# Kernel tuning notes

Measured on AMD Instinct MI355X. Metric: run time of the kernel, lower is better.

Reference implementation:

```python
import jax, jax.numpy as jnp
import numpy as np

NUM_CODES = 8192
DIM = 256
TAU = 1.0
KL_WEIGHT = 0.01
COMMIT_WEIGHT = 0.25
B, C, P = 8, 64, 32


def setup_inputs() -> dict:
    key = jax.random.key(0)
    kz, kc = jax.random.split(key)
    z = jax.random.normal(kz, (B, C, P, DIM), dtype=jnp.float32)
    # nn.init.normal_(codebook.weight, std=1/sqrt(dim))
    codebook = jax.random.normal(kc, (NUM_CODES, DIM), dtype=jnp.float32) / jnp.sqrt(jnp.float32(DIM))
    return {"z": z, "codebook": codebook}


def reference(z, codebook):
    Bq, Cq, Pq, D = z.shape
    flat = z.reshape(-1, D)                                  # (N, D)
    logits = flat @ codebook.T                               # (N, num_codes)
    # training path: gumbel-softmax (hard=False), fixed key for determinism
    g = jax.random.gumbel(jax.random.key(42), logits.shape, dtype=logits.dtype)
    soft_one_hot = jax.nn.softmax((logits + g) / TAU, axis=-1)
    z_q = (soft_one_hot @ codebook).reshape(Bq, Cq, Pq, D)
    # KL to uniform prior: sum(qy * log(qy * K + 1e-10))
    log_qy = jax.nn.log_softmax(logits, axis=-1)
    qy = jnp.exp(log_qy)
    kl_loss = KL_WEIGHT * jnp.mean(jnp.sum(qy * jnp.log(qy * NUM_CODES + 1e-10), axis=-1))
    codes = jnp.argmax(logits, axis=-1).reshape(Bq, Cq, Pq)
    commit_loss = COMMIT_WEIGHT * jnp.mean((jax.lax.stop_gradient(z_q) - z) ** 2)
    z_q_st = z + jax.lax.stop_gradient(z_q - z)              # straight-through
    total_loss = commit_loss + kl_loss
    return (z_q_st, total_loss, codes)
```

## Files before the change

### kernel.cpp

```cpp
#include <hip/hip_runtime.h>
#include <stdint.h>
#include <math.h>

#define N_ROWS   16384
#define N_CODES  8192
#define DIMV     256
#define RT       32
#define CK       32
#define NCHUNK   (N_CODES / CK)
#define CK2      64
#define NITER    (N_CODES / CK2)
#define OUT_ZQ_N ((size_t)N_ROWS * DIMV)
#define OUT_LOSS OUT_ZQ_N
#define OUT_CODE (OUT_ZQ_N + 1)

#define WS_CBHI 0u
#define WS_CBT  4194304u
#define WS_ACC  8388608u
#define WS_NEED (8388608u + 64u)

#define CB1H_OFF  0
#define BSTRIDE   1056
#define P_OFF     33792
#define P_ROW     144
#define S2B_OFF   38400
#define SKL_OFF   38912
#define TKL_OFF   39424
#define SMEM_BYTES 39936
#define ZT_ROWF   260
#define CAND_OFF  0

typedef __attribute__((ext_vector_type(8))) short short8;
typedef __attribute__((ext_vector_type(4))) float float4v;

typedef __attribute__((address_space(1))) uint32_t g_u32;
typedef __attribute__((address_space(3))) uint32_t l_u32;

__device__ __forceinline__ void dma16(const void* gsrc, void* ldst) {
  __builtin_amdgcn_global_load_lds((g_u32*)gsrc, (l_u32*)ldst, 16, 0, 0);
}

__device__ __forceinline__ uint32_t rotl32(uint32_t x, int r) {
  return __builtin_rotateleft32(x, (uint32_t)r);
}

__device__ __forceinline__ uint32_t threefry_bits(uint32_t c) {
  const uint32_t k0 = 0u, k1 = 42u;
  const uint32_t k2 = 0x1BD11BDAu ^ k0 ^ k1;
  uint32_t x0 = 0u + k0;
  uint32_t x1 = c + k1;
#define TF_R(r) { x0 += x1; x1 = rotl32(x1, r); x1 ^= x0; }
  TF_R(13) TF_R(15) TF_R(26) TF_R(6)
  x0 += k1; x1 += k2 + 1u;
  TF_R(17) TF_R(29) TF_R(16) TF_R(24)
  x0 += k2; x1 += k0 + 2u;
  TF_R(13) TF_R(15) TF_R(26) TF_R(6)
  x0 += k0; x1 += k1 + 3u;
  TF_R(17) TF_R(29) TF_R(16) TF_R(24)
  x0 += k1; x1 += k2 + 4u;
  TF_R(13) TF_R(15) TF_R(26) TF_R(6)
  x0 += k2; x1 += k0 + 5u;
#undef TF_R
  return x0 ^ x1;
}

__device__ __forceinline__ float gumbel_at_v1(uint32_t idx) {
  uint32_t bits = threefry_bits(idx);
  float u = __uint_as_float((bits >> 9) | 0x3f800000u) - 1.0f;
  u = fmaxf(u, 1.17549435e-38f);
  return -logf(-logf(u));
}

__device__ __forceinline__ unsigned short f2bf(float x) {
  uint32_t u = __float_as_uint(x);
  u += 0x7fffu + ((u >> 16) & 1u);
  return (unsigned short)(u >> 16);
}
__device__ __forceinline__ float bf2f(unsigned short h) {
  return __uint_as_float(((uint32_t)h) << 16);
}

__global__ __launch_bounds__(256)
void vq_prep(const float* __restrict__ cb, char* __restrict__ ws) {
  __shared__ unsigned short lhs[32 * 260];
  const int c = blockIdx.x;
  const int tid = threadIdx.x;
  const int k0 = c * 32;
  unsigned short* cbhi = (unsigned short*)(ws + WS_CBHI);
  unsigned short* cbt  = (unsigned short*)(ws + WS_CBT);
#pragma unroll
  for (int i = 0; i < 8; ++i) {
    int F = tid + i * 256;
    int code = F >> 6, d4 = (F & 63) * 4;
    float4 v = *(const float4*)(cb + (size_t)(k0 + code) * DIMV + d4);
    unsigned short h0 = f2bf(v.x), h1 = f2bf(v.y), h2 = f2bf(v.z), h3 = f2bf(v.w);
    ushort4 hv = {h0, h1, h2, h3};
    *(ushort4*)(cbhi + (size_t)(k0 + code) * DIMV + d4) = hv;
    *(ushort4*)(&lhs[code * 260 + d4]) = hv;
  }
  __syncthreads();
  const int d = tid;
  unsigned short vals[32];
#pragma unroll
  for (int cc = 0; cc < 32; ++cc) vals[cc] = lhs[cc * 260 + d];
  unsigned short* base = cbt + (size_t)c * 8192 + (size_t)d * 32;
#pragma unroll
  for (int j = 0; j < 8; ++j) {
    ushort4 w = {vals[4 * j], vals[4 * j + 1], vals[4 * j + 2], vals[4 * j + 3]};
    *(ushort4*)(base + j * 4) = w;
  }
}

__global__ __launch_bounds__(512, 4)
void vq_main_v4(const float* __restrict__ z, const float* __restrict__ cb,
                float* __restrict__ out, char* __restrict__ ws) {
  __shared__ __align__(16) char sm[SMEM_BYTES];
  const int tid  = threadIdx.x;
  const int wave = tid >> 6;
  const int lane = tid & 63;
  const int quad = lane >> 4;
  const int n    = lane & 15;
  const int mt   = wave & 1;
  const int nt   = wave >> 1;
  const int r0   = blockIdx.x * RT;
  const int myrow = mt * 16 + quad * 4;
  const char* cbhi_b = ws + WS_CBHI;
  const char* cbt_b  = ws + WS_CBT;
  float* wsA = (float*)(ws + WS_ACC);

  {
    float* zts = (float*)sm;
#pragma unroll
    for (int i = 0; i < 4; ++i) {
      int F = tid + i * 512;
      int row = F >> 6, d4 = (F & 63) * 4;
      *(float4*)(zts + row * ZT_ROWF + d4) =
          *(const float4*)(z + (size_t)(r0 + row) * DIMV + d4);
    }
  }
  __syncthreads();
  short8 zhi[8];
  {
    const float* zts = (const float*)sm;
    const int rowl = mt * 16 + n;
#pragma unroll
    for (int ks = 0; ks < 8; ++ks) {
      const float* zp = zts + rowl * ZT_ROWF + ks * 32 + quad * 8;
      float4 f0 = *(const float4*)zp;
      float4 f1 = *(const float4*)(zp + 4);
      zhi[ks][0] = (short)f2bf(f0.x); zhi[ks][1] = (short)f2bf(f0.y);
      zhi[ks][2] = (short)f2bf(f0.z); zhi[ks][3] = (short)f2bf(f0.w);
      zhi[ks][4] = (short)f2bf(f1.x); zhi[ks][5] = (short)f2bf(f1.y);
      zhi[ks][6] = (short)f2bf(f1.z); zhi[ks][7] = (short)f2bf(f1.w);
    }
  }
  __syncthreads();

#pragma unroll
  for (int i = 0; i < 4; ++i) {
    int b = wave * 4 + i;
    dma16(cbhi_b + (size_t)(2 * b) * 512 + (size_t)lane * 16, sm + CB1H_OFF + b * BSTRIDE);
  }
  __syncthreads();

  float skl[4] = {0.f, 0.f, 0.f, 0.f};
  float tkl[4] = {0.f, 0.f, 0.f, 0.f};
  float s2l[4] = {0.f, 0.f, 0.f, 0.f};
  float v1[4], v2[4];
  int   i1[4], i2[4];
#pragma unroll
  for (int r = 0; r < 4; ++r) {
    v1[r] = -INFINITY; v2[r] = -INFINITY;
    i1[r] = 0x7fffffff; i2[r] = 0x7fffffff;
  }
  const int kc = nt * 16 + n;
  uint32_t idxA = (uint32_t)(r0 + myrow) * (uint32_t)N_CODES + (uint32_t)kc;
  float4v acc2[4];
#pragma unroll
  for (int t = 0; t < 4; ++t) acc2[t] = (float4v){0.f, 0.f, 0.f, 0.f};

  const char* bbase = sm + CB1H_OFF + (kc >> 1) * BSTRIDE + (kc & 1) * 512 + quad * 16;
  const char* g2base = cbt_b + ((size_t)(wave * 32 + n) * 32 + (size_t)(quad * 8)) * 2;

  for (int c = 0; c < NITER; ++c) {
    float4v e0 = (float4v){0.f, 0.f, 0.f, 0.f};
    float4v e1 = (float4v){0.f, 0.f, 0.f, 0.f};
#pragma unroll
    for (int ks = 0; ks < 4; ++ks) {
      short8 ba  = *(const short8*)(bbase + (2 * ks) * 64);
      short8 bbv = *(const short8*)(bbase + (2 * ks + 1) * 64);
      e0 = __builtin_amdgcn_mfma_f32_16x16x32_bf16(zhi[2 * ks], ba, e0, 0, 0, 0);
      e1 = __builtin_amdgcn_mfma_f32_16x16x32_bf16(zhi[2 * ks + 1], bbv, e1, 0, 0, 0);
    }
    float4v acc1 = e0 + e1;

    __syncthreads();

    if (c + 1 < NITER) {
      const size_t k1 = (size_t)(c + 1) * CK2;
#pragma unroll
      for (int i = 0; i < 4; ++i) {
        int b = wave * 4 + i;
        dma16(cbhi_b + (k1 + 2 * b) * 512 + (size_t)lane * 16, sm + CB1H_OFF + b * BSTRIDE);
      }
    }
    const char* gc = g2base + (size_t)(2 * c) * 16384;
    short8 bb00 = *(const short8*)(gc);
    short8 bb01 = *(const short8*)(gc + 1024);
    short8 bb10 = *(const short8*)(gc + 16384);
    short8 bb11 = *(const short8*)(gc + 16384 + 1024);

    const int codeg0 = c * CK2 + kc;
    uint32_t bits4[4];
#pragma unroll
    for (int r = 0; r < 4; ++r)
      bits4[r] = threefry_bits(idxA + (uint32_t)r * (uint32_t)N_CODES);
#pragma unroll
    for (int r = 0; r < 4; ++r) {
      float l = acc1[r];
      uint32_t bits = bits4[r];
      float u = __uint_as_float((bits >> 9) | 0x3f800000u) - 1.0f;
      float t = -0.69314718056f * __log2f(fmaxf(u, 1.17549435e-38f));
      t = fmaxf(t, 1.0e-10f);
      float e = __expf(l);
      skl[r] += e;
      tkl[r] = fmaf(e, l, tkl[r]);
      bool b1 = l > v1[r];
      bool b2 = l > v2[r];
      v2[r] = b1 ? v1[r] : (b2 ? l : v2[r]);
      i2[r] = b1 ? i1[r] : (b2 ? codeg0 : i2[r]);
      v1[r] = b1 ? l : v1[r];
      i1[r] = b1 ? codeg0 : i1[r];
      float p = e * __builtin_amdgcn_rcpf(t) * 6.1442123533282097e-06f;
      unsigned short ph = f2bf(p);
      s2l[r] += bf2f(ph);
      *(unsigned short*)(sm + P_OFF + (myrow + r) * P_ROW + kc * 2) = ph;
    }
    idxA += (uint32_t)CK2;

    __syncthreads();

    {
      short8 pa00 = *(const short8*)(sm + P_OFF + n * P_ROW + quad * 16);
      short8 pa01 = *(const short8*)(sm + P_OFF + n * P_ROW + 64 + quad * 16);
      short8 pa10 = *(const short8*)(sm + P_OFF + (16 + n) * P_ROW + quad * 16);
      short8 pa11 = *(const short8*)(sm + P_OFF + (16 + n) * P_ROW + 64 + quad * 16);
      acc2[0] = __builtin_amdgcn_mfma_f32_16x16x32_bf16(pa00, bb00, acc2[0], 0, 0, 0);
      acc2[0] = __builtin_amdgcn_mfma_f32_16x16x32_bf16(pa01, bb10, acc2[0], 0, 0, 0);
      acc2[1] = __builtin_amdgcn_mfma_f32_16x16x32_bf16(pa00, bb01, acc2[1], 0, 0, 0);
      acc2[1] = __builtin_amdgcn_mfma_f32_16x16x32_bf16(pa01, bb11, acc2[1], 0, 0, 0);
      acc2[2] = __builtin_amdgcn_mfma_f32_16x16x32_bf16(pa10, bb00, acc2[2], 0, 0, 0);
      acc2[2] = __builtin_amdgcn_mfma_f32_16x16x32_bf16(pa11, bb10, acc2[2], 0, 0, 0);
      acc2[3] = __builtin_amdgcn_mfma_f32_16x16x32_bf16(pa10, bb01, acc2[3], 0, 0, 0);
      acc2[3] = __builtin_amdgcn_mfma_f32_16x16x32_bf16(pa11, bb11, acc2[3], 0, 0, 0);
    }
  }

#pragma unroll
  for (int m = 1; m <= 8; m <<= 1) {
#pragma unroll
    for (int r = 0; r < 4; ++r) {
      s2l[r] += __shfl_xor(s2l[r], m);
      skl[r] += __shfl_xor(skl[r], m);
      tkl[r] += __shfl_xor(tkl[r], m);
    }
  }
  if (n == 0) {
    int off = nt * 128 + myrow * 4;
    float4 fs = {s2l[0], s2l[1], s2l[2], s2l[3]};
    *(float4*)(sm + S2B_OFF + off) = fs;
    float4 fk = {skl[0], skl[1], skl[2], skl[3]};
    *(float4*)(sm + SKL_OFF + off) = fk;
    float4 ft = {tkl[0], tkl[1], tkl[2], tkl[3]};
    *(float4*)(sm + TKL_OFF + off) = ft;
  }
#pragma unroll
  for (int r = 0; r < 4; ++r) {
    char* cbase = sm + CAND_OFF + (myrow + r) * 1024 + kc * 16;
    *(float*)(cbase + 0) = v1[r];
    *(int*)(cbase + 4)   = i1[r];
    *(float*)(cbase + 8) = v2[r];
    *(int*)(cbase + 12)  = i2[r];
  }
  __syncthreads();

  if (tid < 32) {
    int r = tid;
    const float* sklb = (const float*)(sm + SKL_OFF);
    const float* tklb = (const float*)(sm + TKL_OFF);
    float S = (sklb[r] + sklb[32 + r]) + (sklb[64 + r] + sklb[96 + r]);
    float T = (tklb[r] + tklb[32 + r]) + (tklb[64 + r] + tklb[96 + r]);
    float klr = T / S - __logf(S) + 9.010913347279288f;
#pragma unroll
    for (int m = 1; m <= 16; m <<= 1) klr += __shfl_xor(klr, m);
    if (r == 0) atomicAdd(&wsA[0], klr);
  }

  if (tid < 64) {
    int r = tid >> 1, h = tid & 1;
    const char* cbase = sm + CAND_OFF + r * 1024 + h * 512;
    float bv[8]; int bi8[8];
#pragma unroll
    for (int k = 0; k < 8; ++k) { bv[k] = -INFINITY; bi8[k] = 0x7fffffff; }
    for (int s = 0; s < 64; ++s) {
      float v = *(const float*)(cbase + s * 8);
      int  id = *(const int*)(cbase + s * 8 + 4);
      if ((v > bv[7]) || (v == bv[7] && id < bi8[7])) {
        float cv = v; int ci = id;
#pragma unroll
        for (int k = 0; k < 8; ++k) {
          bool sw = (cv > bv[k]) || (cv == bv[k] && ci < bi8[k]);
          float tv = bv[k]; int ti = bi8[k];
          if (sw) { bv[k] = cv; bi8[k] = ci; cv = tv; ci = ti; }
        }
      }
    }
    float ovv[8]; int ovi[8];
#pragma unroll
    for (int k = 0; k < 8; ++k) {
      ovv[k] = __shfl_xor(bv[k], 1);
      ovi[k] = __shfl_xor(bi8[k], 1);
    }
#pragma unroll
    for (int kk = 0; kk < 8; ++kk) {
      float cv = ovv[kk]; int ci = ovi[kk];
      if ((cv > bv[7]) || (cv == bv[7] && ci < bi8[7])) {
#pragma unroll
        for (int k = 0; k < 8; ++k) {
          bool sw = (cv > bv[k]) || (cv == bv[k] && ci < bi8[k]);
          float tv = bv[k]; int ti = bi8[k];
          if (sw) { bv[k] = cv; bi8[k] = ci; cv = tv; ci = ti; }
        }
      }
    }
    const float* zp = z + (size_t)(r0 + r) * DIMV;
    double best = -1.0e300;
    int bidx = 0x7fffffff;
#pragma unroll
    for (int k = 0; k < 4; ++k) {
      int cidx = bi8[h * 4 + k];
      const float* cp = cb + (size_t)cidx * DIMV;
      double d = 0.0;
      for (int dd = 0; dd < DIMV; dd += 4) {
        float4 zv = *(const float4*)(zp + dd);
        float4 xv = *(const float4*)(cp + dd);
        d += (double)zv.x * xv.x + (double)zv.y * xv.y +
             (double)zv.z * xv.z + (double)zv.w * xv.w;
      }
      if (d > best || (d == best && cidx < bidx)) { best = d; bidx = cidx; }
    }
    double obest = __shfl_xor(best, 1);
    int    obidx = __shfl_xor(bidx, 1);
    bool take = (obest > best) || (obest == best && obidx < bidx);
    int finali = take ? obidx : bidx;
    if (h == 0) out[OUT_CODE + (size_t)(r0 + r)] = (float)finali;
  }

  float invm0[4], invm1[4];
  {
    const float* s2b = (const float*)(sm + S2B_OFF);
#pragma unroll
    for (int e = 0; e < 4; ++e) {
      int ra = quad * 4 + e, rb = 16 + quad * 4 + e;
      float Sa = (s2b[ra] + s2b[32 + ra]) + (s2b[64 + ra] + s2b[96 + ra]);
      float Sb = (s2b[rb] + s2b[32 + rb]) + (s2b[64 + rb] + s2b[96 + rb]);
      invm0[e] = 1.0f / Sa;
      invm1[e] = 1.0f / Sb;
    }
  }
  float cpart = 0.f;
#pragma unroll
  for (int t = 0; t < 2; ++t) {
    int dim = wave * 32 + t * 16 + n;
#pragma unroll
    for (int ms = 0; ms < 2; ++ms) {
      float4v a = acc2[ms * 2 + t];
#pragma unroll
      for (int e = 0; e < 4; ++e) {
        int row = ms * 16 + quad * 4 + e;
        float q = a[e] * (ms ? invm1[e] : invm0[e]);
        float zv = z[(size_t)(r0 + row) * DIMV + dim];
        float err = q - zv;
        cpart += err * err;
        out[(size_t)(r0 + row) * DIMV + dim] = zv + err;
      }
    }
  }
#pragma unroll
  for (int m = 1; m <= 32; m <<= 1) cpart += __shfl_xor(cpart, m);
  if (lane == 0) atomicAdd(&wsA[1], cpart);
}

#define ZSTRIDE  260
#define CSTRIDE  260
#define PSTRIDE  36
#define RSTRIDE  17

__global__ __launch_bounds__(256, 2)
void vq_main_v1(const float* __restrict__ z, const float* __restrict__ cb,
                float* __restrict__ out, float* __restrict__ ws_acc) {
  __shared__ float zt[RT * ZSTRIDE];
  __shared__ float cbt[CK * CSTRIDE];
  __shared__ float ptile[RT * PSTRIDE];
  __shared__ float redb[RT * RSTRIDE];
  __shared__ float m2s[RT], s2s[RT], scls[RT];

  const int tid = threadIdx.x;
  const int r0  = blockIdx.x * RT;
#pragma unroll
  for (int p = 0; p < 8; ++p) {
    int q = tid + p * 256;
    int i = q >> 6, c4 = (q & 63) * 4;
    *(float4*)(&zt[i * ZSTRIDE + c4]) = *(const float4*)(z + (size_t)(r0 + i) * DIMV + c4);
  }
  if (tid < RT) { m2s[tid] = -INFINITY; s2s[tid] = 0.f; scls[tid] = 0.f; }
  const int tr = tid & 15, tk = tid >> 4, rowg = tid >> 6;
  const int d4 = (tid & 63) * 4;
  float c_m[2][2], c_s[2][2], c_t[2][2];
  int   c_i[2][2];
#pragma unroll
  for (int a = 0; a < 2; ++a)
#pragma unroll
    for (int b = 0; b < 2; ++b) { c_m[a][b] = -INFINITY; c_s[a][b] = 0.f; c_t[a][b] = 0.f; c_i[a][b] = 0; }
  float acc2[8][4];
#pragma unroll
  for (int j = 0; j < 8; ++j)
#pragma unroll
    for (int e = 0; e < 4; ++e) acc2[j][e] = 0.f;
  __syncthreads();
  for (int c = 0; c < NCHUNK; ++c) {
    const int k0 = c * CK;
#pragma unroll
    for (int p = 0; p < 8; ++p) {
      int q = tid + p * 256;
      int i = q >> 6, c4 = (q & 63) * 4;
      *(float4*)(&cbt[i * CSTRIDE + c4]) = *(const float4*)(cb + (size_t)(k0 + i) * DIMV + c4);
    }
    __syncthreads();
    float l00 = 0.f, l01 = 0.f, l10 = 0.f, l11 = 0.f;
    {
      const float* zp0 = &zt[tr * ZSTRIDE];
      const float* zp1 = &zt[(tr + 16) * ZSTRIDE];
      const float* bp0 = &cbt[tk * CSTRIDE];
      const float* bp1 = &cbt[(tk + 16) * CSTRIDE];
#pragma unroll 4
      for (int d = 0; d < DIMV; d += 4) {
        float4 a0 = *(const float4*)(zp0 + d);
        float4 a1 = *(const float4*)(zp1 + d);
        float4 b0 = *(const float4*)(bp0 + d);
        float4 b1 = *(const float4*)(bp1 + d);
        l00 += a0.x*b0.x + a0.y*b0.y + a0.z*b0.z + a0.w*b0.w;
        l01 += a0.x*b1.x + a0.y*b1.y + a0.z*b1.z + a0.w*b1.w;
        l10 += a1.x*b0.x + a1.y*b0.y + a1.z*b0.z + a1.w*b0.w;
        l11 += a1.x*b1.x + a1.y*b1.y + a1.z*b1.z + a1.w*b1.w;
      }
    }
    float lv2[2][2] = {{l00, l01}, {l10, l11}};
    float a2[2][2];
#pragma unroll
    for (int a = 0; a < 2; ++a) {
      int grow = r0 + tr + a * 16;
#pragma unroll
      for (int b = 0; b < 2; ++b) {
        int gk = k0 + tk + b * 16;
        float g  = gumbel_at_v1((uint32_t)grow * (uint32_t)N_CODES + (uint32_t)gk);
        float lv = lv2[a][b];
        a2[a][b] = lv + g;
        if (lv > c_m[a][b]) {
          float sc = expf(c_m[a][b] - lv);
          c_s[a][b] = c_s[a][b] * sc + 1.0f;
          c_t[a][b] = c_t[a][b] * sc + lv;
          c_m[a][b] = lv;
          c_i[a][b] = gk;
        } else {
          float e = expf(lv - c_m[a][b]);
          c_s[a][b] += e;
          c_t[a][b] += e * lv;
        }
      }
    }
    redb[tr * RSTRIDE + tk]        = fmaxf(a2[0][0], a2[0][1]);
    redb[(tr + 16) * RSTRIDE + tk] = fmaxf(a2[1][0], a2[1][1]);
    __syncthreads();
    if (tid < RT) {
      float cm = -INFINITY;
#pragma unroll
      for (int j = 0; j < 16; ++j) cm = fmaxf(cm, redb[tid * RSTRIDE + j]);
      float m2n = fmaxf(m2s[tid], cm);
      scls[tid] = expf(m2s[tid] - m2n);
      m2s[tid]  = m2n;
    }
    __syncthreads();
#pragma unroll
    for (int a = 0; a < 2; ++a) {
      int row = tr + a * 16;
      float m2r = m2s[row];
      float p0 = expf(a2[a][0] - m2r);
      float p1 = expf(a2[a][1] - m2r);
      ptile[row * PSTRIDE + tk]      = p0;
      ptile[row * PSTRIDE + tk + 16] = p1;
      redb[row * RSTRIDE + tk] = p0 + p1;
    }
    __syncthreads();
    if (tid < RT) {
      float ss = 0.f;
#pragma unroll
      for (int j = 0; j < 16; ++j) ss += redb[tid * RSTRIDE + j];
      s2s[tid] = s2s[tid] * scls[tid] + ss;
    }
#pragma unroll
    for (int j = 0; j < 8; ++j) {
      float sc = scls[rowg * 8 + j];
      acc2[j][0] *= sc; acc2[j][1] *= sc; acc2[j][2] *= sc; acc2[j][3] *= sc;
    }
    for (int k4 = 0; k4 < CK; k4 += 4) {
      float4 cb0 = *(const float4*)(&cbt[(k4 + 0) * CSTRIDE + d4]);
      float4 cb1v = *(const float4*)(&cbt[(k4 + 1) * CSTRIDE + d4]);
      float4 cb2 = *(const float4*)(&cbt[(k4 + 2) * CSTRIDE + d4]);
      float4 cb3 = *(const float4*)(&cbt[(k4 + 3) * CSTRIDE + d4]);
#pragma unroll
      for (int j = 0; j < 8; ++j) {
        float4 p4 = *(const float4*)(&ptile[(rowg * 8 + j) * PSTRIDE + k4]);
        acc2[j][0] += p4.x*cb0.x + p4.y*cb1v.x + p4.z*cb2.x + p4.w*cb3.x;
        acc2[j][1] += p4.x*cb0.y + p4.y*cb1v.y + p4.z*cb2.y + p4.w*cb3.y;
        acc2[j][2] += p4.x*cb0.z + p4.y*cb1v.z + p4.z*cb2.z + p4.w*cb3.z;
        acc2[j][3] += p4.x*cb0.w + p4.y*cb1v.w + p4.z*cb2.w + p4.w*cb3.w;
      }
    }
    __syncthreads();
  }
  float* kbuf = cbt;
#pragma unroll
  for (int a = 0; a < 2; ++a) {
    float m0 = c_m[a][0], m1v = c_m[a][1];
    float m, s, t; int bi;
    if (m0 >= m1v) {
      float e = expf(m1v - m0);
      m = m0; s = c_s[a][0] + c_s[a][1] * e; t = c_t[a][0] + c_t[a][1] * e;
    } else {
      float e = expf(m0 - m1v);
      m = m1v; s = c_s[a][0] * e + c_s[a][1]; t = c_t[a][0] * e + c_t[a][1];
    }
    if (m0 > m1v)      bi = c_i[a][0];
    else if (m1v > m0) bi = c_i[a][1];
    else               bi = min(c_i[a][0], c_i[a][1]);
    int row = tr + a * 16;
    kbuf[row * 65 + tk * 4 + 0] = m;
    kbuf[row * 65 + tk * 4 + 1] = s;
    kbuf[row * 65 + tk * 4 + 2] = t;
    kbuf[row * 65 + tk * 4 + 3] = (float)bi;
  }
  __syncthreads();
  if (tid < RT) {
    int r = tid;
    float M = -INFINITY, S = 0.f, T = 0.f, BM = -INFINITY;
    int BI = 0x7fffffff;
    for (int j = 0; j < 16; ++j) {
      float m  = kbuf[r * 65 + j * 4 + 0];
      float s  = kbuf[r * 65 + j * 4 + 1];
      float t  = kbuf[r * 65 + j * 4 + 2];
      int   bi = (int)kbuf[r * 65 + j * 4 + 3];
      if (m <= M) {
        float e = expf(m - M);
        S += s * e; T += t * e;
      } else {
        float e = expf(M - m);
        S = S * e + s; T = T * e + t; M = m;
      }
      if (m > BM || (m == BM && bi < BI)) { BM = m; BI = bi; }
    }
    float kl = logf((float)N_CODES) + T / S - M - logf(S);
    atomicAdd(&ws_acc[0], kl);
    out[OUT_CODE + (size_t)(r0 + r)] = (float)BI;
  }
  float cpart = 0.f;
#pragma unroll
  for (int j = 0; j < 8; ++j) {
    int row  = rowg * 8 + j;
    int grow = r0 + row;
    float inv = 1.0f / s2s[row];
    float4 zv = *(const float4*)(&zt[row * ZSTRIDE + d4]);
    float q0 = acc2[j][0] * inv, q1 = acc2[j][1] * inv;
    float q2 = acc2[j][2] * inv, q3 = acc2[j][3] * inv;
    float e0 = q0 - zv.x, e1 = q1 - zv.y, e2 = q2 - zv.z, e3 = q3 - zv.w;
    cpart += e0*e0 + e1*e1 + e2*e2 + e3*e3;
    float4 o;
    o.x = zv.x + e0; o.y = zv.y + e1; o.z = zv.z + e2; o.w = zv.w + e3;
    *(float4*)(&out[(size_t)grow * DIMV + d4]) = o;
  }
#pragma unroll
  for (int off = 32; off > 0; off >>= 1) cpart += __shfl_down(cpart, off, 64);
  __syncthreads();
  if ((tid & 63) == 0) redb[tid >> 6] = cpart;
  __syncthreads();
  if (tid == 0) {
    float cs = redb[0] + redb[1] + redb[2] + redb[3];
    atomicAdd(&ws_acc[1], cs);
  }
}

__global__ void vq_finalize(const float* __restrict__ ws_acc, float* __restrict__ out) {
  if (threadIdx.x == 0 && blockIdx.x == 0) {
    float kl = 0.01f * (ws_acc[0] / (float)N_ROWS);
    float cm = 0.25f * (ws_acc[1] / (float)OUT_ZQ_N);
    out[OUT_LOSS] = cm + kl;
  }
}

extern "C" void kernel_launch(void* const* d_in, const int* in_sizes, int n_in,
                              void* d_out, int out_size, void* d_ws, size_t ws_size,
                              hipStream_t stream) {
  (void)in_sizes; (void)n_in; (void)out_size;
  const float* z  = (const float*)d_in[0];
  const float* cb = (const float*)d_in[1];
  float* out = (float*)d_out;
  if (ws_size >= (size_t)WS_NEED) {
    char* ws = (char*)d_ws;
    hipMemsetAsync(ws + WS_ACC, 0, 8, stream);
    vq_prep<<<256, 256, 0, stream>>>(cb, ws);
    vq_main_v4<<<N_ROWS / RT, 512, 0, stream>>>(z, cb, out, ws);
    vq_finalize<<<1, 64, 0, stream>>>((const float*)(ws + WS_ACC), out);
  } else {
    float* ws = (float*)d_ws;
    hipMemsetAsync(ws, 0, 8, stream);
    vq_main_v1<<<N_ROWS / RT, 256, 0, stream>>>(z, cb, out, ws);
    vq_finalize<<<1, 64, 0, stream>>>(ws, out);
  }
}
```

Before: 665.0 us.

## Double-buffer codebook and probability tiles in LDS to drop a barrier

The codebook-half LDS tile and the probability tile each get two buffers that alternate by iteration parity. This removes one of the two __syncthreads per iteration, so the next chunk's DMA can overlap with the current chunk's compute. Odd blocks also sleep briefly at start to stagger their phase against even blocks. The cost is roughly double the LDS per block (about 78KB), which may cut occupancy from the launch-bound target of 4 blocks per CU. Correctness rests on the single remaining barrier ordering all buffer reuse.

```diff
diff --git a/kernel.cpp b/kernel.cpp
--- a/kernel.cpp
+++ b/kernel.cpp
@@ -19,14 +19,17 @@
 #define WS_ACC  8388608u
 #define WS_NEED (8388608u + 64u)
 
-#define CB1H_OFF  0
+#define CBH0_OFF  0
+#define CBH1_OFF  33792
+#define CBH_SZ    33792
 #define BSTRIDE   1056
-#define P_OFF     33792
+#define P0_OFF    67584
+#define P_BUF_SZ  4608
 #define P_ROW     144
-#define S2B_OFF   38400
-#define SKL_OFF   38912
-#define TKL_OFF   39424
-#define SMEM_BYTES 39936
+#define S2B_OFF   76800
+#define SKL_OFF   77312
+#define TKL_OFF   77824
+#define SMEM_BYTES 78336
 #define ZT_ROWF   260
 #define CAND_OFF  0
 
@@ -112,9 +115,12 @@
 }
 
 __global__ __launch_bounds__(512, 4)
-void vq_main_v4(const float* __restrict__ z, const float* __restrict__ cb,
+void vq_main_v5(const float* __restrict__ z, const float* __restrict__ cb,
                 float* __restrict__ out, char* __restrict__ ws) {
   __shared__ __align__(16) char sm[SMEM_BYTES];
+
+  if (blockIdx.x & 1) __builtin_amdgcn_s_sleep(80);
+
   const int tid  = threadIdx.x;
   const int wave = tid >> 6;
   const int lane = tid & 63;
@@ -159,7 +165,7 @@
 #pragma unroll
   for (int i = 0; i < 4; ++i) {
     int b = wave * 4 + i;
-    dma16(cbhi_b + (size_t)(2 * b) * 512 + (size_t)lane * 16, sm + CB1H_OFF + b * BSTRIDE);
+    dma16(cbhi_b + (size_t)(2 * b) * 512 + (size_t)lane * 16, sm + CBH0_OFF + b * BSTRIDE);
   }
   __syncthreads();
 
@@ -179,10 +185,13 @@
 #pragma unroll
   for (int t = 0; t < 4; ++t) acc2[t] = (float4v){0.f, 0.f, 0.f, 0.f};
 
-  const char* bbase = sm + CB1H_OFF + (kc >> 1) * BSTRIDE + (kc & 1) * 512 + quad * 16;
+  const char* bbase0 = sm + CBH0_OFF + (kc >> 1) * BSTRIDE + (kc & 1) * 512 + quad * 16;
   const char* g2base = cbt_b + ((size_t)(wave * 32 + n) * 32 + (size_t)(quad * 8)) * 2;
 
   for (int c = 0; c < NITER; ++c) {
+    const int par = c & 1;
+
+    const char* bbase = bbase0 + par * CBH_SZ;
     float4v e0 = (float4v){0.f, 0.f, 0.f, 0.f};
     float4v e1 = (float4v){0.f, 0.f, 0.f, 0.f};
 #pragma unroll
@@ -194,14 +203,13 @@
     }
     float4v acc1 = e0 + e1;
 
-    __syncthreads();
-
     if (c + 1 < NITER) {
       const size_t k1 = (size_t)(c + 1) * CK2;
+      char* dst = sm + (par ? CBH0_OFF : CBH1_OFF);
 #pragma unroll
       for (int i = 0; i < 4; ++i) {
         int b = wave * 4 + i;
-        dma16(cbhi_b + (k1 + 2 * b) * 512 + (size_t)lane * 16, sm + CB1H_OFF + b * BSTRIDE);
+        dma16(cbhi_b + (k1 + 2 * b) * 512 + (size_t)lane * 16, dst + b * BSTRIDE);
       }
     }
     const char* gc = g2base + (size_t)(2 * c) * 16384;
@@ -211,6 +219,7 @@
     short8 bb11 = *(const short8*)(gc + 16384 + 1024);
 
     const int codeg0 = c * CK2 + kc;
+    char* pw = sm + P0_OFF + par * P_BUF_SZ;
     uint32_t bits4[4];
 #pragma unroll
     for (int r = 0; r < 4; ++r)
@@ -234,17 +243,18 @@
       float p = e * __builtin_amdgcn_rcpf(t) * 6.1442123533282097e-06f;
       unsigned short ph = f2bf(p);
       s2l[r] += bf2f(ph);
-      *(unsigned short*)(sm + P_OFF + (myrow + r) * P_ROW + kc * 2) = ph;
+      *(unsigned short*)(pw + (myrow + r) * P_ROW + kc * 2) = ph;
     }
     idxA += (uint32_t)CK2;
 
     __syncthreads();
 
     {
-      short8 pa00 = *(const short8*)(sm + P_OFF + n * P_ROW + quad * 16);
-      short8 pa01 = *(const short8*)(sm + P_OFF + n * P_ROW + 64 + quad * 16);
-      short8 pa10 = *(const short8*)(sm + P_OFF + (16 + n) * P_ROW + quad * 16);
-      short8 pa11 = *(const short8*)(sm + P_OFF + (16 + n) * P_ROW + 64 + quad * 16);
+      const char* pr = sm + P0_OFF + par * P_BUF_SZ;
+      short8 pa00 = *(const short8*)(pr + n * P_ROW + quad * 16);
+      short8 pa01 = *(const short8*)(pr + n * P_ROW + 64 + quad * 16);
+      short8 pa10 = *(const short8*)(pr + (16 + n) * P_ROW + quad * 16);
+      short8 pa11 = *(const short8*)(pr + (16 + n) * P_ROW + 64 + quad * 16);
       acc2[0] = __builtin_amdgcn_mfma_f32_16x16x32_bf16(pa00, bb00, acc2[0], 0, 0, 0);
       acc2[0] = __builtin_amdgcn_mfma_f32_16x16x32_bf16(pa01, bb10, acc2[0], 0, 0, 0);
       acc2[1] = __builtin_amdgcn_mfma_f32_16x16x32_bf16(pa00, bb01, acc2[1], 0, 0, 0);
@@ -618,7 +628,7 @@
     char* ws = (char*)d_ws;
     hipMemsetAsync(ws + WS_ACC, 0, 8, stream);
     vq_prep<<<256, 256, 0, stream>>>(cb, ws);
-    vq_main_v4<<<N_ROWS / RT, 512, 0, stream>>>(z, cb, out, ws);
+    vq_main_v5<<<N_ROWS / RT, 512, 0, stream>>>(z, cb, out, ws);
     vq_finalize<<<1, 64, 0, stream>>>((const float*)(ws + WS_ACC), out);
   } else {
     float* ws = (float*)d_ws;
```

Result: faster. 639.9 us (-3.8%).
